# Kernel optimization log

Hardware: AMD Instinct MI355X
Metric: run time of the kernel (lower is better)

The kernel has to match this reference:

```python
import jax, jax.numpy as jnp
import numpy as np

B, N, C = 256, 256, 128   # batch (=N_res rows), seq len, pair channels
H, D = 4, 128             # heads, per-head dim (== output_dim per module code)
O = 128                   # output_dim


def _glorot(key, shape, fan_in, fan_out):
    limit = np.sqrt(6.0 / (fan_in + fan_out))
    return jax.random.uniform(key, shape, jnp.float32, -limit, limit)


def setup_inputs() -> dict:
    key = jax.random.key(0)
    ks = jax.random.split(key, 9)
    q_data = jax.random.normal(ks[0], (B, N, C), jnp.float32)
    m_data = jax.random.normal(ks[1], (B, N, C), jnp.float32)
    bias = jax.random.normal(ks[2], (B, 1, N, N), jnp.float32)
    nonbatched_bias = jax.random.normal(ks[3], (H, N, N), jnp.float32)
    query_w = _glorot(ks[4], (C, H, D), C, H * D)
    key_w = _glorot(ks[5], (C, H, D), C, H * D)
    value_w = _glorot(ks[6], (C, H, D), C, H * D)
    gating_w = jnp.zeros((C, H, D), jnp.float32)
    gating_b = jnp.ones((H, D), jnp.float32)
    output_w = _glorot(ks[7], (H, D, O), H * D, O)
    output_b = jnp.zeros((O,), jnp.float32)
    return {
        'q_data': q_data, 'm_data': m_data, 'bias': bias,
        'nonbatched_bias': nonbatched_bias,
        'query_w': query_w, 'key_w': key_w, 'value_w': value_w,
        'gating_w': gating_w, 'gating_b': gating_b,
        'output_w': output_w, 'output_b': output_b,
    }


def reference(q_data, m_data, bias, nonbatched_bias,
              query_w, key_w, value_w, gating_w, gating_b,
              output_w, output_b):
    key_dim = query_w.shape[-1]  # per-head dim (tied to output_dim in module)
    q = jnp.einsum('bqa,ahc->bqhc', q_data, query_w) * key_dim ** (-0.5)
    k = jnp.einsum('bka,ahc->bkhc', m_data, key_w)
    v = jnp.einsum('bka,ahc->bkhc', m_data, value_w)
    logits = jnp.einsum('bqhc,bkhc->bhqk', q, k) + bias
    logits = logits + nonbatched_bias[None]  # broadcast shared bias over batch
    weights = jax.nn.softmax(logits, axis=-1)
    weighted_avg = jnp.einsum('bhqk,bkhc->bqhc', weights, v)
    gate = jax.nn.sigmoid(jnp.einsum('bqc,chv->bqhv', q_data, gating_w) + gating_b)
    weighted_avg = weighted_avg * gate
    return jnp.einsum('bqhc,hco->bqo', weighted_avg, output_w) + output_b
```

## Files before the change

kernel.cpp:

```cpp
#include <hip/hip_runtime.h>
#include <stdint.h>


typedef unsigned short u16;
typedef u16 u16x8 __attribute__((ext_vector_type(8)));
typedef u16 u16x4 __attribute__((ext_vector_type(4)));
typedef __bf16 bf16x8 __attribute__((ext_vector_type(8)));
typedef float floatx4 __attribute__((ext_vector_type(4)));

union B8 { u16x8 u; bf16x8 b; };

__device__ __forceinline__ float bf2f(u16 u) {
  union { uint32_t i; float f; } v; v.i = ((uint32_t)u) << 16; return v.f;
}
__device__ __forceinline__ u16 f2bf(float f) {
  union { float f; uint32_t i; } v; v.f = f;
  return (u16)((v.i + 0x7fffu + ((v.i >> 16) & 1u)) >> 16);
}
__device__ __forceinline__ bf16x8 ld8(const u16* p) { return *(const bf16x8*)p; }
__device__ __forceinline__ floatx4 mfma16(bf16x8 a, bf16x8 b, floatx4 c) {
  return __builtin_amdgcn_mfma_f32_16x16x32_bf16(a, b, c, 0, 0, 0);
}
__device__ __forceinline__ void cfence() { asm volatile("" ::: "memory"); }

template<bool BF>
__device__ __forceinline__ bf16x8 ldin8(const void* p, long long idx) {
  if constexpr (BF) {
    return *(const bf16x8*)((const u16*)p + idx);
  } else {
    const float* f = (const float*)p + idx;
    floatx4 a = *(const floatx4*)f;
    floatx4 b = *(const floatx4*)(f + 4);
    B8 r;
    #pragma unroll
    for (int i = 0; i < 4; ++i) { r.u[i] = f2bf(a[i]); r.u[i + 4] = f2bf(b[i]); }
    return r.b;
  }
}
template<bool BF>
__device__ __forceinline__ float ldin1(const void* p, long long idx) {
  if constexpr (BF) return bf2f(((const u16*)p)[idx]);
  else              return ((const float*)p)[idx];
}

template<bool BF>
__device__ __forceinline__ void pre_body(
    const void* bias, const void* nbias,
    const void* qw, const void* kw, const void* vw, const void* gw,
    const void* ow, u16* wt, u16* b16, u16* nb16)
{
  const int blk = blockIdx.x, tid = threadIdx.x;
  if (blk < 4160) {
    const void* src = (blk < 4096) ? bias : nbias;
    u16* dst = (blk < 4096) ? b16 : nb16;
    long long base = (long long)((blk < 4096) ? blk : blk - 4096) * 4096;
    #pragma unroll
    for (int it = 0; it < 4; ++it) {
      long long idx = base + it * 1024 + tid * 4;
      if constexpr (BF) {
        *(u16x4*)(dst + idx) = *(const u16x4*)((const u16*)src + idx);
      } else {
        floatx4 v = *(const floatx4*)((const float*)src + idx);
        u16x4 o;
        #pragma unroll
        for (int i = 0; i < 4; ++i) o[i] = f2bf(v[i]);
        *(u16x4*)(dst + idx) = o;
      }
    }
  } else if (blk < 4176) {
    const int mh = blk - 4160, mat = mh >> 2, h = mh & 3;
    const void* W = (mat == 0) ? qw : (mat == 1) ? kw : (mat == 2) ? vw : gw;
    u16* dst = wt + mh * 16384;
    for (int idx = tid; idx < 16384; idx += 256) {
      int c = idx >> 7, d = idx & 127;
      dst[d * 128 + c] = f2bf(ldin1<BF>(W, (long long)c * 512 + h * 128 + d));
    }
  } else {
    const int part = blk - 4176;
    u16* dst = wt + 16 * 16384;
    for (int idx = tid; idx < 16384; idx += 256) {
      int k = idx >> 7, o = idx & 127;
      int kg = part * 128 + k;
      dst[o * 512 + kg] = f2bf(ldin1<BF>(ow, (long long)kg * 128 + o));
    }
  }
}

__global__ __launch_bounds__(256) void k_pre(
    const void* bias, const void* nbias,
    const void* qw, const void* kw, const void* vw, const void* gw,
    const void* ow, const void* gating_b, u16* wt, u16* b16, u16* nb16)
{
  const bool bf = (*(const uint32_t*)gating_b) == 0x3F803F80u;
  if (bf) pre_body<true >(bias, nbias, qw, kw, vw, gw, ow, wt, b16, nb16);
  else    pre_body<false>(bias, nbias, qw, kw, vw, gw, ow, wt, b16, nb16);
}

template<bool BF>
__device__ __forceinline__ void proj_body(
    const void* q_data, const void* m_data,
    const u16* wt, u16* reg, int b0, int Bc)
{
  const int tid  = threadIdx.x;
  const int lane = tid & 63, w = tid >> 6;
  const int quad = lane >> 4, l15 = lane & 15;
  const int mat  = blockIdx.y >> 2, h = blockIdx.y & 3;
  const int r0l  = blockIdx.x * 128;
  const int bl   = r0l >> 8, n0 = r0l & 255;
  const int bg   = b0 + bl;
  const long long regElems = (long long)Bc * 131072;

  const void* src = (mat == 0) ? q_data : m_data;
  const u16*  Wt  = wt + (mat * 4 + h) * 16384;

  const int wm = w >> 1, wn = w & 1;
  floatx4 acc[4][4];
  #pragma unroll
  for (int mi = 0; mi < 4; ++mi)
    #pragma unroll
    for (int ni = 0; ni < 4; ++ni)
      acc[mi][ni] = (floatx4){0.f, 0.f, 0.f, 0.f};

  #pragma unroll
  for (int ks = 0; ks < 4; ++ks) {
    bf16x8 af[4], bw[4];
    #pragma unroll
    for (int mi = 0; mi < 4; ++mi) {
      long long row = (long long)bg * 256 + n0 + wm * 64 + mi * 16 + l15;
      af[mi] = ldin8<BF>(src, row * 128 + ks * 32 + quad * 8);
    }
    #pragma unroll
    for (int ni = 0; ni < 4; ++ni) {
      int col = wn * 64 + ni * 16 + l15;
      bw[ni] = ld8(Wt + col * 128 + ks * 32 + quad * 8);
    }
    #pragma unroll
    for (int mi = 0; mi < 4; ++mi)
      #pragma unroll
      for (int ni = 0; ni < 4; ++ni)
        acc[mi][ni] = mfma16(af[mi], bw[ni], acc[mi][ni]);
  }

  const float scale = 0.088388347648318447f;
  const long long bh = (long long)(bl * 4 + h);
  #pragma unroll
  for (int mi = 0; mi < 4; ++mi) {
    #pragma unroll
    for (int ni = 0; ni < 4; ++ni) {
      if (mat == 2) {
        int j = wn * 64 + ni * 16 + l15;
        int i0 = wm * 64 + mi * 16 + quad * 4;
        u16x4 v4;
        #pragma unroll
        for (int r = 0; r < 4; ++r) v4[r] = f2bf(acc[mi][ni][r]);
        *(u16x4*)(reg + 2 * regElems + (bh * 128 + j) * 256 + (n0 + i0)) = v4;
      } else {
        #pragma unroll
        for (int r = 0; r < 4; ++r) {
          int i = wm * 64 + mi * 16 + quad * 4 + r;
          int j = wn * 64 + ni * 16 + l15;
          float v = acc[mi][ni][r];
          if (mat == 0) v *= scale;
          reg[(long long)mat * regElems + (bh * 256 + (n0 + i)) * 128 + j] = f2bf(v);
        }
      }
    }
  }
}

__global__ __launch_bounds__(256) void k_proj(
    const void* q_data, const void* m_data, const void* gating_b,
    const u16* wt, u16* reg, int b0, int Bc)
{
  const bool bf = (*(const uint32_t*)gating_b) == 0x3F803F80u;
  if (bf) proj_body<true >(q_data, m_data, wt, reg, b0, Bc);
  else    proj_body<false>(q_data, m_data, wt, reg, b0, Bc);
}

template<bool BF>
__device__ __forceinline__ void attn_body(
    const void* q_data, const u16* __restrict__ b16,
    const u16* __restrict__ nb16, const void* gating_b,
    const u16* __restrict__ wt, u16* reg, int b0, int Bc, char* smem)
{
  const int tid  = threadIdx.x;
  const int lane = tid & 63, w = tid >> 6;
  const int quad = lane >> 4, l15 = lane & 15;
  const int bl = blockIdx.x, h = blockIdx.y, qt = blockIdx.z;
  const int bg = b0 + bl;
  const int m0 = qt * 64 + w * 16;
  const long long regElems = (long long)Bc * 131072;
  const long long bh = (long long)(bl * 4 + h);

  const u16* Qb = reg;
  const u16* Kb = reg + regElems     + bh * 32768;
  const u16* Vt = reg + 2 * regElems + bh * 32768;
  u16*       Ob = reg + 3 * regElems;
  const u16* wtG = wt + (3 * 4 + h) * 16384;

  char* scr = smem + w * 4352;

  bf16x8 aq[4];
  #pragma unroll
  for (int ks = 0; ks < 4; ++ks)
    aq[ks] = ld8(Qb + (bh * 256 + m0 + l15) * 128 + ks * 32 + quad * 8);

  floatx4 s[16];
  #pragma unroll
  for (int nt = 0; nt < 16; ++nt) s[nt] = (floatx4){0.f, 0.f, 0.f, 0.f};

  #pragma unroll
  for (int kc = 0; kc < 4; ++kc) {
    float* sBf = (float*)scr;
    #pragma unroll
    for (int it = 0; it < 4; ++it) {
      int slot = it * 64 + lane;
      int row = slot >> 4, c4 = (slot & 15) << 2;
      long long gi = ((long long)bg * 256 + m0 + row) * 256 + kc * 64 + c4;
      long long ni = ((long long)h  * 256 + m0 + row) * 256 + kc * 64 + c4;
      u16x4 bu = *(const u16x4*)(b16 + gi);
      u16x4 nu = *(const u16x4*)(nb16 + ni);
      floatx4 v;
      #pragma unroll
      for (int i = 0; i < 4; ++i) v[i] = bf2f(bu[i]) + bf2f(nu[i]);
      *(floatx4*)(sBf + row * 68 + c4) = v;
    }
    #pragma unroll
    for (int ntl = 0; ntl < 4; ++ntl) {
      const int nt = kc * 4 + ntl;
      #pragma unroll
      for (int ks = 0; ks < 4; ++ks) {
        bf16x8 bk = ld8(Kb + (kc * 64 + ntl * 16 + l15) * 128 + ks * 32 + quad * 8);
        s[nt] = mfma16(aq[ks], bk, s[nt]);
      }
      #pragma unroll
      for (int r = 0; r < 4; ++r)
        s[nt][r] += sBf[(quad * 4 + r) * 68 + ntl * 16 + l15];
    }
    cfence();
  }

  float mx[4] = {-1e30f, -1e30f, -1e30f, -1e30f};
  #pragma unroll
  for (int nt = 0; nt < 16; ++nt)
    #pragma unroll
    for (int r = 0; r < 4; ++r) mx[r] = fmaxf(mx[r], s[nt][r]);
  #pragma unroll
  for (int r = 0; r < 4; ++r)
    #pragma unroll
    for (int off = 1; off < 16; off <<= 1)
      mx[r] = fmaxf(mx[r], __shfl_xor(mx[r], off));
  float sm[4] = {0.f, 0.f, 0.f, 0.f};
  #pragma unroll
  for (int nt = 0; nt < 16; ++nt)
    #pragma unroll
    for (int r = 0; r < 4; ++r) {
      float e = __expf(s[nt][r] - mx[r]);
      s[nt][r] = e; sm[r] += e;
    }
  #pragma unroll
  for (int r = 0; r < 4; ++r)
    #pragma unroll
    for (int off = 1; off < 16; off <<= 1)
      sm[r] += __shfl_xor(sm[r], off);
  float inv[4];
  #pragma unroll
  for (int r = 0; r < 4; ++r) inv[r] = 1.f / sm[r];

  u16* sPw = (u16*)scr;
  floatx4 o[8];
  #pragma unroll
  for (int dt = 0; dt < 8; ++dt) o[dt] = (floatx4){0.f, 0.f, 0.f, 0.f};
  #pragma unroll
  for (int half = 0; half < 2; ++half) {
    #pragma unroll
    for (int ntl = 0; ntl < 8; ++ntl)
      #pragma unroll
      for (int r = 0; r < 4; ++r)
        sPw[(quad * 4 + r) * 136 + ntl * 16 + l15] =
            f2bf(s[half * 8 + ntl][r] * inv[r]);
    bf16x8 ap[4];
    #pragma unroll
    for (int ks = 0; ks < 4; ++ks)
      ap[ks] = ld8(sPw + l15 * 136 + ks * 32 + quad * 8);
    #pragma unroll
    for (int dt = 0; dt < 8; ++dt)
      #pragma unroll
      for (int ks = 0; ks < 4; ++ks) {
        bf16x8 bv = ld8(Vt + (dt * 16 + l15) * 256 + half * 128 + ks * 32 + quad * 8);
        o[dt] = mfma16(ap[ks], bv, o[dt]);
      }
    cfence();
  }

  bf16x8 aqd[4];
  #pragma unroll
  for (int ks = 0; ks < 4; ++ks)
    aqd[ks] = ldin8<BF>(q_data, ((long long)bg * 256 + m0 + l15) * 128 + ks * 32 + quad * 8);
  #pragma unroll
  for (int nt = 0; nt < 8; ++nt) {
    floatx4 g = (floatx4){0.f, 0.f, 0.f, 0.f};
    #pragma unroll
    for (int ks = 0; ks < 4; ++ks) {
      bf16x8 bw = ld8(wtG + (nt * 16 + l15) * 128 + ks * 32 + quad * 8);
      g = mfma16(aqd[ks], bw, g);
    }
    #pragma unroll
    for (int r = 0; r < 4; ++r) {
      int row = m0 + quad * 4 + r, d = nt * 16 + l15;
      float gate = 1.f / (1.f + __expf(-(g[r] + ldin1<BF>(gating_b, h * 128 + d))));
      Ob[(bh * 256 + row) * 128 + d] = f2bf(o[nt][r] * gate);
    }
  }
}

__global__ __launch_bounds__(256, 4) void k_attn(
    const void* q_data, const u16* b16, const u16* nb16,
    const void* gating_b, const u16* wt, u16* reg, int b0, int Bc)
{
  __shared__ __align__(16) char smem[17408];
  const bool bf = (*(const uint32_t*)gating_b) == 0x3F803F80u;
  if (bf) attn_body<true >(q_data, b16, nb16, gating_b, wt, reg, b0, Bc, smem);
  else    attn_body<false>(q_data, b16, nb16, gating_b, wt, reg, b0, Bc, smem);
}

template<bool BF>
__device__ __forceinline__ void out_body(
    const u16* wsr, const u16* wtO, const void* output_b,
    void* out, int b0)
{
  const int tid  = threadIdx.x;
  const int lane = tid & 63, w = tid >> 6;
  const int quad = lane >> 4, l15 = lane & 15;
  const int wm = w >> 1, wn = w & 1;
  const int r0l = blockIdx.x * 32;
  const int bl  = r0l >> 8, n0 = r0l & 255;

  floatx4 acc[4];
  #pragma unroll
  for (int ni = 0; ni < 4; ++ni) acc[ni] = (floatx4){0.f, 0.f, 0.f, 0.f};

  #pragma unroll
  for (int kt = 0; kt < 4; ++kt) {
    #pragma unroll
    for (int ks = 0; ks < 4; ++ks) {
      bf16x8 af = ld8(wsr + ((long long)(bl * 4 + kt) * 256 + n0 + wm * 16 + l15) * 128
                          + ks * 32 + quad * 8);
      #pragma unroll
      for (int ni = 0; ni < 4; ++ni) {
        int col = wn * 64 + ni * 16 + l15;
        bf16x8 bw = ld8(wtO + (long long)col * 512 + kt * 128 + ks * 32 + quad * 8);
        acc[ni] = mfma16(af, bw, acc[ni]);
      }
    }
  }

  #pragma unroll
  for (int ni = 0; ni < 4; ++ni) {
    #pragma unroll
    for (int r = 0; r < 4; ++r) {
      int i = wm * 16 + quad * 4 + r;
      int j = wn * 64 + ni * 16 + l15;
      long long orow = (long long)b0 * 256 + r0l + i;
      float v = acc[ni][r] + ldin1<BF>(output_b, j);
      if constexpr (BF) ((u16*)out)[orow * 128 + j] = f2bf(v);
      else              ((float*)out)[orow * 128 + j] = v;
    }
  }
}

__global__ __launch_bounds__(256) void k_out(
    const u16* wsr, const u16* wtO, const void* output_b,
    const void* gating_b, void* out, int b0)
{
  const bool bf = (*(const uint32_t*)gating_b) == 0x3F803F80u;
  if (bf) out_body<true >(wsr, wtO, output_b, out, b0);
  else    out_body<false>(wsr, wtO, output_b, out, b0);
}

extern "C" void kernel_launch(void* const* d_in, const int* in_sizes, int n_in,
                              void* d_out, int out_size, void* d_ws, size_t ws_size,
                              hipStream_t stream)
{
  (void)in_sizes; (void)n_in; (void)out_size;
  const void* q_data   = d_in[0];
  const void* m_data   = d_in[1];
  const void* bias     = d_in[2];
  const void* nbias    = d_in[3];
  const void* query_w  = d_in[4];
  const void* key_w    = d_in[5];
  const void* value_w  = d_in[6];
  const void* gating_w = d_in[7];
  const void* gating_b = d_in[8];
  const void* output_w = d_in[9];
  const void* output_b = d_in[10];
  u16* ws = (u16*)d_ws;

  const long long wtElems  = 16 * 16384 + 128 * 512;
  const long long b16Elems = 256LL * 256 * 256;
  const long long nbElems  = 4LL * 256 * 256;
  const long long fixedElems = wtElems + b16Elems + nbElems;
  u16* wt   = ws;
  u16* wtO  = wt + 16 * 16384;
  u16* b16  = ws + wtElems;
  u16* nb16 = b16 + b16Elems;
  u16* reg  = ws + fixedElems;

  const size_t per_batch_bytes = 4ull * 131072 * 2;
  const size_t fixed_bytes = (size_t)fixedElems * 2;
  int Bc = 1;
  while (Bc * 2 <= 256 &&
         fixed_bytes + (size_t)(Bc * 2) * per_batch_bytes <= ws_size) Bc *= 2;

  k_pre<<<4180, 256, 0, stream>>>(bias, nbias, query_w, key_w, value_w,
                                  gating_w, output_w, gating_b, wt, b16, nb16);

  const long long regElems = (long long)Bc * 131072;
  for (int b0 = 0; b0 < 256; b0 += Bc) {
    dim3 g1(2 * Bc, 12);
    k_proj<<<g1, 256, 0, stream>>>(q_data, m_data, gating_b, wt, reg, b0, Bc);
    dim3 g2(Bc, 4, 4);
    k_attn<<<g2, 256, 0, stream>>>(q_data, b16, nb16, gating_b, wt, reg, b0, Bc);
    dim3 g3(8 * Bc);
    k_out<<<g3, 256, 0, stream>>>(reg + 3 * regElems, wtO, output_b,
                                  gating_b, d_out, b0);
  }
}
```

Measured before the change: 775.0 us.

## Read bias directly in attention instead of pre-converting to bf16 workspace

Removes the pre-pass that converted the full 64MB fp32 bias to a bf16 copy in workspace, and instead has the attention kernel load the bias in its native dtype directly. This eliminates a full read+write pass over the largest input, at the cost of the attention kernel reading fp32 (twice the bytes of the bf16 copy). It also flattens the attention grid to 1D with an XCD-style swizzle of block ids so that neighbouring work lands on the same chiplet, and frees workspace, which may allow a larger batch chunk.

```diff
diff --git a/kernel.cpp b/kernel.cpp
--- a/kernel.cpp
+++ b/kernel.cpp
@@ -45,30 +45,28 @@
 
 template<bool BF>
 __device__ __forceinline__ void pre_body(
-    const void* bias, const void* nbias,
+    const void* nbias,
     const void* qw, const void* kw, const void* vw, const void* gw,
-    const void* ow, u16* wt, u16* b16, u16* nb16)
+    const void* ow, u16* wt, u16* nb16)
 {
   const int blk = blockIdx.x, tid = threadIdx.x;
-  if (blk < 4160) {
-    const void* src = (blk < 4096) ? bias : nbias;
-    u16* dst = (blk < 4096) ? b16 : nb16;
-    long long base = (long long)((blk < 4096) ? blk : blk - 4096) * 4096;
+  if (blk < 64) {
+    long long base = (long long)blk * 4096;
     #pragma unroll
     for (int it = 0; it < 4; ++it) {
       long long idx = base + it * 1024 + tid * 4;
       if constexpr (BF) {
-        *(u16x4*)(dst + idx) = *(const u16x4*)((const u16*)src + idx);
+        *(u16x4*)(nb16 + idx) = *(const u16x4*)((const u16*)nbias + idx);
       } else {
-        floatx4 v = *(const floatx4*)((const float*)src + idx);
+        floatx4 v = *(const floatx4*)((const float*)nbias + idx);
         u16x4 o;
         #pragma unroll
         for (int i = 0; i < 4; ++i) o[i] = f2bf(v[i]);
-        *(u16x4*)(dst + idx) = o;
-      }
-    }
-  } else if (blk < 4176) {
-    const int mh = blk - 4160, mat = mh >> 2, h = mh & 3;
+        *(u16x4*)(nb16 + idx) = o;
+      }
+    }
+  } else if (blk < 80) {
+    const int mh = blk - 64, mat = mh >> 2, h = mh & 3;
     const void* W = (mat == 0) ? qw : (mat == 1) ? kw : (mat == 2) ? vw : gw;
     u16* dst = wt + mh * 16384;
     for (int idx = tid; idx < 16384; idx += 256) {
@@ -76,7 +74,7 @@
       dst[d * 128 + c] = f2bf(ldin1<BF>(W, (long long)c * 512 + h * 128 + d));
     }
   } else {
-    const int part = blk - 4176;
+    const int part = blk - 80;
     u16* dst = wt + 16 * 16384;
     for (int idx = tid; idx < 16384; idx += 256) {
       int k = idx >> 7, o = idx & 127;
@@ -87,13 +85,13 @@
 }
 
 __global__ __launch_bounds__(256) void k_pre(
-    const void* bias, const void* nbias,
+    const void* nbias,
     const void* qw, const void* kw, const void* vw, const void* gw,
-    const void* ow, const void* gating_b, u16* wt, u16* b16, u16* nb16)
+    const void* ow, const void* gating_b, u16* wt, u16* nb16)
 {
   const bool bf = (*(const uint32_t*)gating_b) == 0x3F803F80u;
-  if (bf) pre_body<true >(bias, nbias, qw, kw, vw, gw, ow, wt, b16, nb16);
-  else    pre_body<false>(bias, nbias, qw, kw, vw, gw, ow, wt, b16, nb16);
+  if (bf) pre_body<true >(nbias, qw, kw, vw, gw, ow, wt, nb16);
+  else    pre_body<false>(nbias, qw, kw, vw, gw, ow, wt, nb16);
 }
 
 template<bool BF>
@@ -179,14 +177,20 @@
 
 template<bool BF>
 __device__ __forceinline__ void attn_body(
-    const void* q_data, const u16* __restrict__ b16,
+    const void* q_data, const void* __restrict__ bias,
     const u16* __restrict__ nb16, const void* gating_b,
     const u16* __restrict__ wt, u16* reg, int b0, int Bc, char* smem)
 {
   const int tid  = threadIdx.x;
   const int lane = tid & 63, w = tid >> 6;
   const int quad = lane >> 4, l15 = lane & 15;
-  const int bl = blockIdx.x, h = blockIdx.y, qt = blockIdx.z;
+
+  const int nwg = Bc * 16;
+  const int id  = blockIdx.x;
+  const int per = nwg >> 3;
+  const int swz = (id & 7) * per + (id >> 3);
+  const int bl = swz >> 4, h = (swz >> 2) & 3, qt = swz & 3;
+
   const int bg = b0 + bl;
   const int m0 = qt * 64 + w * 16;
   const long long regElems = (long long)Bc * 131072;
@@ -218,11 +222,17 @@
       int row = slot >> 4, c4 = (slot & 15) << 2;
       long long gi = ((long long)bg * 256 + m0 + row) * 256 + kc * 64 + c4;
       long long ni = ((long long)h  * 256 + m0 + row) * 256 + kc * 64 + c4;
-      u16x4 bu = *(const u16x4*)(b16 + gi);
       u16x4 nu = *(const u16x4*)(nb16 + ni);
       floatx4 v;
-      #pragma unroll
-      for (int i = 0; i < 4; ++i) v[i] = bf2f(bu[i]) + bf2f(nu[i]);
+      if constexpr (BF) {
+        u16x4 bu = *(const u16x4*)((const u16*)bias + gi);
+        #pragma unroll
+        for (int i = 0; i < 4; ++i) v[i] = bf2f(bu[i]) + bf2f(nu[i]);
+      } else {
+        floatx4 bv = *(const floatx4*)((const float*)bias + gi);
+        #pragma unroll
+        for (int i = 0; i < 4; ++i) v[i] = bv[i] + bf2f(nu[i]);
+      }
       *(floatx4*)(sBf + row * 68 + c4) = v;
     }
     #pragma unroll
@@ -315,13 +325,13 @@
 }
 
 __global__ __launch_bounds__(256, 4) void k_attn(
-    const void* q_data, const u16* b16, const u16* nb16,
+    const void* q_data, const void* bias, const u16* nb16,
     const void* gating_b, const u16* wt, u16* reg, int b0, int Bc)
 {
   __shared__ __align__(16) char smem[17408];
   const bool bf = (*(const uint32_t*)gating_b) == 0x3F803F80u;
-  if (bf) attn_body<true >(q_data, b16, nb16, gating_b, wt, reg, b0, Bc, smem);
-  else    attn_body<false>(q_data, b16, nb16, gating_b, wt, reg, b0, Bc, smem);
+  if (bf) attn_body<true >(q_data, bias, nb16, gating_b, wt, reg, b0, Bc, smem);
+  else    attn_body<false>(q_data, bias, nb16, gating_b, wt, reg, b0, Bc, smem);
 }
 
 template<bool BF>
@@ -397,13 +407,11 @@
   u16* ws = (u16*)d_ws;
 
   const long long wtElems  = 16 * 16384 + 128 * 512;
-  const long long b16Elems = 256LL * 256 * 256;
   const long long nbElems  = 4LL * 256 * 256;
-  const long long fixedElems = wtElems + b16Elems + nbElems;
+  const long long fixedElems = wtElems + nbElems;
   u16* wt   = ws;
   u16* wtO  = wt + 16 * 16384;
-  u16* b16  = ws + wtElems;
-  u16* nb16 = b16 + b16Elems;
+  u16* nb16 = ws + wtElems;
   u16* reg  = ws + fixedElems;
 
   const size_t per_batch_bytes = 4ull * 131072 * 2;
@@ -412,15 +420,15 @@
   while (Bc * 2 <= 256 &&
          fixed_bytes + (size_t)(Bc * 2) * per_batch_bytes <= ws_size) Bc *= 2;
 
-  k_pre<<<4180, 256, 0, stream>>>(bias, nbias, query_w, key_w, value_w,
-                                  gating_w, output_w, gating_b, wt, b16, nb16);
+  k_pre<<<84, 256, 0, stream>>>(nbias, query_w, key_w, value_w,
+                                gating_w, output_w, gating_b, wt, nb16);
 
   const long long regElems = (long long)Bc * 131072;
   for (int b0 = 0; b0 < 256; b0 += Bc) {
     dim3 g1(2 * Bc, 12);
     k_proj<<<g1, 256, 0, stream>>>(q_data, m_data, gating_b, wt, reg, b0, Bc);
-    dim3 g2(Bc, 4, 4);
-    k_attn<<<g2, 256, 0, stream>>>(q_data, b16, nb16, gating_b, wt, reg, b0, Bc);
+    k_attn<<<Bc * 16, 256, 0, stream>>>(q_data, bias, nb16, gating_b, wt,
+                                        reg, b0, Bc);
     dim3 g3(8 * Bc);
     k_out<<<g3, 256, 0, stream>>>(reg + 3 * regElems, wtO, output_b,
                                   gating_b, d_out, b0);
```

After: 769.3 us. About the same (-0.7%).

## Fuse QKV projection, attention and gating into one kernel with LDS-resident K/V

Applied to the files above, without the earlier changes.

Merges the projection and attention kernels into a single 512-thread workgroup per (batch, head). It computes Q, K and V on chip, keeps K and transposed V in swizzled LDS, and reads the fp32 bias and nonbatched bias directly instead of pre-converting them to bf16 in a separate pass. This removes the global round trip of Q/K/V, the big bias conversion kernel, and one launch per chunk. It also adds an XCD-aware block swizzle and defers the softmax normalisation to the output. In exchange it uses about 146KB of LDS per block, which limits occupancy, and it issues scalar fp32 bias loads.

```diff
diff --git a/kernel.cpp b/kernel.cpp
--- a/kernel.cpp
+++ b/kernel.cpp
@@ -45,38 +45,20 @@
 
 template<bool BF>
 __device__ __forceinline__ void pre_body(
-    const void* bias, const void* nbias,
     const void* qw, const void* kw, const void* vw, const void* gw,
-    const void* ow, u16* wt, u16* b16, u16* nb16)
+    const void* ow, u16* wt)
 {
   const int blk = blockIdx.x, tid = threadIdx.x;
-  if (blk < 4160) {
-    const void* src = (blk < 4096) ? bias : nbias;
-    u16* dst = (blk < 4096) ? b16 : nb16;
-    long long base = (long long)((blk < 4096) ? blk : blk - 4096) * 4096;
-    #pragma unroll
-    for (int it = 0; it < 4; ++it) {
-      long long idx = base + it * 1024 + tid * 4;
-      if constexpr (BF) {
-        *(u16x4*)(dst + idx) = *(const u16x4*)((const u16*)src + idx);
-      } else {
-        floatx4 v = *(const floatx4*)((const float*)src + idx);
-        u16x4 o;
-        #pragma unroll
-        for (int i = 0; i < 4; ++i) o[i] = f2bf(v[i]);
-        *(u16x4*)(dst + idx) = o;
-      }
-    }
-  } else if (blk < 4176) {
-    const int mh = blk - 4160, mat = mh >> 2, h = mh & 3;
+  if (blk < 16) {
+    const int mat = blk >> 2, h = blk & 3;
     const void* W = (mat == 0) ? qw : (mat == 1) ? kw : (mat == 2) ? vw : gw;
-    u16* dst = wt + mh * 16384;
+    u16* dst = wt + blk * 16384;
     for (int idx = tid; idx < 16384; idx += 256) {
       int c = idx >> 7, d = idx & 127;
       dst[d * 128 + c] = f2bf(ldin1<BF>(W, (long long)c * 512 + h * 128 + d));
     }
   } else {
-    const int part = blk - 4176;
+    const int part = blk - 16;
     u16* dst = wt + 16 * 16384;
     for (int idx = tid; idx < 16384; idx += 256) {
       int k = idx >> 7, o = idx & 127;
@@ -87,241 +69,256 @@
 }
 
 __global__ __launch_bounds__(256) void k_pre(
-    const void* bias, const void* nbias,
     const void* qw, const void* kw, const void* vw, const void* gw,
-    const void* ow, const void* gating_b, u16* wt, u16* b16, u16* nb16)
+    const void* ow, const void* gating_b, u16* wt)
 {
   const bool bf = (*(const uint32_t*)gating_b) == 0x3F803F80u;
-  if (bf) pre_body<true >(bias, nbias, qw, kw, vw, gw, ow, wt, b16, nb16);
-  else    pre_body<false>(bias, nbias, qw, kw, vw, gw, ow, wt, b16, nb16);
+  if (bf) pre_body<true >(qw, kw, vw, gw, ow, wt);
+  else    pre_body<false>(qw, kw, vw, gw, ow, wt);
 }
 
 template<bool BF>
-__device__ __forceinline__ void proj_body(
+__device__ __forceinline__ void fused_body(
     const void* q_data, const void* m_data,
-    const u16* wt, u16* reg, int b0, int Bc)
+    const void* __restrict__ bias, const void* __restrict__ nbias,
+    const void* gating_b, const u16* __restrict__ wt,
+    u16* Ob, int b0, int Bc, u16* smem)
 {
   const int tid  = threadIdx.x;
   const int lane = tid & 63, w = tid >> 6;
   const int quad = lane >> 4, l15 = lane & 15;
-  const int mat  = blockIdx.y >> 2, h = blockIdx.y & 3;
-  const int r0l  = blockIdx.x * 128;
-  const int bl   = r0l >> 8, n0 = r0l & 255;
-  const int bg   = b0 + bl;
-  const long long regElems = (long long)Bc * 131072;
-
-  const void* src = (mat == 0) ? q_data : m_data;
-  const u16*  Wt  = wt + (mat * 4 + h) * 16384;
-
-  const int wm = w >> 1, wn = w & 1;
-  floatx4 acc[4][4];
+  const int l7   = l15 & 7;
+
+  const int nwg = Bc * 4, id = blockIdx.x;
+  const int xcd = id & 7, rest = id >> 3;
+  const int qq = nwg >> 3, rm = nwg & 7;
+  const int swz = (xcd < rm ? xcd * (qq + 1) : rm * (qq + 1) + (xcd - rm) * qq) + rest;
+  const int bl = swz >> 2, h = swz & 3;
+  const int bg = b0 + bl;
+  const long long bh = (long long)(bl * 4 + h);
+
+  u16* Kl  = smem;
+  u16* Vtl = Kl + 32768;
+  u16* sPw = Vtl + 32768 + w * 1152;
+
+  const u16* wtQ = wt + (0 * 4 + h) * 16384;
+  const u16* wtK = wt + (1 * 4 + h) * 16384;
+  const u16* wtV = wt + (2 * 4 + h) * 16384;
+  const u16* wtG = wt + (3 * 4 + h) * 16384;
+  const float scale = 0.088388347648318447f;
+
+  bf16x8 aq[2][4];
+  u16* Qs = Kl + w * 4096;
   #pragma unroll
-  for (int mi = 0; mi < 4; ++mi)
-    #pragma unroll
-    for (int ni = 0; ni < 4; ++ni)
-      acc[mi][ni] = (floatx4){0.f, 0.f, 0.f, 0.f};
+  for (int p = 0; p < 2; ++p) {
+    const int m0 = p * 128 + w * 16;
+    floatx4 qa[8];
+    #pragma unroll
+    for (int ni = 0; ni < 8; ++ni) qa[ni] = (floatx4){0.f, 0.f, 0.f, 0.f};
+    #pragma unroll
+    for (int ks = 0; ks < 4; ++ks) {
+      bf16x8 aA = ldin8<BF>(q_data, ((long long)bg * 256 + m0 + l15) * 128 + ks * 32 + quad * 8);
+      #pragma unroll
+      for (int ni = 0; ni < 8; ++ni) {
+        bf16x8 bw = ld8(wtQ + (ni * 16 + l15) * 128 + ks * 32 + quad * 8);
+        qa[ni] = mfma16(aA, bw, qa[ni]);
+      }
+    }
+    #pragma unroll
+    for (int ni = 0; ni < 8; ++ni)
+      #pragma unroll
+      for (int r = 0; r < 4; ++r)
+        Qs[(quad * 4 + r) * 136 + ni * 16 + l15] = f2bf(qa[ni][r] * scale);
+    cfence();
+    #pragma unroll
+    for (int ks = 0; ks < 4; ++ks)
+      aq[p][ks] = ld8(Qs + l15 * 136 + ks * 32 + quad * 8);
+    cfence();
+  }
+  __syncthreads();
+
+  const int nb = w * 32;
+  {
+    floatx4 ka[2][8];
+    #pragma unroll
+    for (int mi = 0; mi < 2; ++mi)
+      #pragma unroll
+      for (int ni = 0; ni < 8; ++ni) ka[mi][ni] = (floatx4){0.f, 0.f, 0.f, 0.f};
+    #pragma unroll
+    for (int ks = 0; ks < 4; ++ks) {
+      bf16x8 bw[8];
+      #pragma unroll
+      for (int ni = 0; ni < 8; ++ni)
+        bw[ni] = ld8(wtK + (ni * 16 + l15) * 128 + ks * 32 + quad * 8);
+      #pragma unroll
+      for (int mi = 0; mi < 2; ++mi) {
+        bf16x8 aA = ldin8<BF>(m_data, ((long long)bg * 256 + nb + mi * 16 + l15) * 128 + ks * 32 + quad * 8);
+        #pragma unroll
+        for (int ni = 0; ni < 8; ++ni)
+          ka[mi][ni] = mfma16(aA, bw[ni], ka[mi][ni]);
+      }
+    }
+    #pragma unroll
+    for (int mi = 0; mi < 2; ++mi)
+      #pragma unroll
+      for (int ni = 0; ni < 8; ++ni)
+        #pragma unroll
+        for (int r = 0; r < 4; ++r) {
+          int n = nb + mi * 16 + quad * 4 + r;
+          int d = ni * 16 + l15;
+          Kl[n * 128 + (d ^ ((n & 7) << 3))] = f2bf(ka[mi][ni][r]);
+        }
+  }
+  {
+    floatx4 va[2][8];
+    #pragma unroll
+    for (int mi = 0; mi < 2; ++mi)
+      #pragma unroll
+      for (int ni = 0; ni < 8; ++ni) va[mi][ni] = (floatx4){0.f, 0.f, 0.f, 0.f};
+    #pragma unroll
+    for (int ks = 0; ks < 4; ++ks) {
+      bf16x8 bw[8];
+      #pragma unroll
+      for (int ni = 0; ni < 8; ++ni)
+        bw[ni] = ld8(wtV + (ni * 16 + l15) * 128 + ks * 32 + quad * 8);
+      #pragma unroll
+      for (int mi = 0; mi < 2; ++mi) {
+        bf16x8 aA = ldin8<BF>(m_data, ((long long)bg * 256 + nb + mi * 16 + l15) * 128 + ks * 32 + quad * 8);
+        #pragma unroll
+        for (int ni = 0; ni < 8; ++ni)
+          va[mi][ni] = mfma16(aA, bw[ni], va[mi][ni]);
+      }
+    }
+    #pragma unroll
+    for (int mi = 0; mi < 2; ++mi)
+      #pragma unroll
+      for (int ni = 0; ni < 8; ++ni) {
+        int d = ni * 16 + l15;
+        int n4 = nb + mi * 16 + quad * 4;
+        u16x4 v4;
+        #pragma unroll
+        for (int r = 0; r < 4; ++r) v4[r] = f2bf(va[mi][ni][r]);
+        *(u16x4*)(Vtl + d * 256 + (n4 ^ ((d & 7) << 3))) = v4;
+      }
+  }
+  __syncthreads();
 
   #pragma unroll
-  for (int ks = 0; ks < 4; ++ks) {
-    bf16x8 af[4], bw[4];
-    #pragma unroll
-    for (int mi = 0; mi < 4; ++mi) {
-      long long row = (long long)bg * 256 + n0 + wm * 64 + mi * 16 + l15;
-      af[mi] = ldin8<BF>(src, row * 128 + ks * 32 + quad * 8);
-    }
-    #pragma unroll
-    for (int ni = 0; ni < 4; ++ni) {
-      int col = wn * 64 + ni * 16 + l15;
-      bw[ni] = ld8(Wt + col * 128 + ks * 32 + quad * 8);
-    }
-    #pragma unroll
-    for (int mi = 0; mi < 4; ++mi)
-      #pragma unroll
-      for (int ni = 0; ni < 4; ++ni)
-        acc[mi][ni] = mfma16(af[mi], bw[ni], acc[mi][ni]);
-  }
-
-  const float scale = 0.088388347648318447f;
-  const long long bh = (long long)(bl * 4 + h);
-  #pragma unroll
-  for (int mi = 0; mi < 4; ++mi) {
-    #pragma unroll
-    for (int ni = 0; ni < 4; ++ni) {
-      if (mat == 2) {
-        int j = wn * 64 + ni * 16 + l15;
-        int i0 = wm * 64 + mi * 16 + quad * 4;
-        u16x4 v4;
-        #pragma unroll
-        for (int r = 0; r < 4; ++r) v4[r] = f2bf(acc[mi][ni][r]);
-        *(u16x4*)(reg + 2 * regElems + (bh * 128 + j) * 256 + (n0 + i0)) = v4;
-      } else {
+  for (int p = 0; p < 2; ++p) {
+    const int m0 = p * 128 + w * 16;
+
+    floatx4 s[16];
+    #pragma unroll
+    for (int nt = 0; nt < 16; ++nt) s[nt] = (floatx4){0.f, 0.f, 0.f, 0.f};
+    #pragma unroll
+    for (int kc = 0; kc < 4; ++kc) {
+      float bz[4][4];
+      #pragma unroll
+      for (int ntl = 0; ntl < 4; ++ntl)
         #pragma unroll
         for (int r = 0; r < 4; ++r) {
-          int i = wm * 64 + mi * 16 + quad * 4 + r;
-          int j = wn * 64 + ni * 16 + l15;
-          float v = acc[mi][ni][r];
-          if (mat == 0) v *= scale;
-          reg[(long long)mat * regElems + (bh * 256 + (n0 + i)) * 128 + j] = f2bf(v);
+          long long gi = ((long long)bg * 256 + m0 + quad * 4 + r) * 256 + kc * 64 + ntl * 16 + l15;
+          long long gn = ((long long)h * 256 + m0 + quad * 4 + r) * 256 + kc * 64 + ntl * 16 + l15;
+          bz[ntl][r] = ldin1<BF>(bias, gi) + ldin1<BF>(nbias, gn);
         }
-      }
-    }
-  }
-}
-
-__global__ __launch_bounds__(256) void k_proj(
-    const void* q_data, const void* m_data, const void* gating_b,
-    const u16* wt, u16* reg, int b0, int Bc)
-{
+      #pragma unroll
+      for (int ntl = 0; ntl < 4; ++ntl) {
+        const int nt = kc * 4 + ntl;
+        #pragma unroll
+        for (int ks = 0; ks < 4; ++ks) {
+          bf16x8 bk = ld8(Kl + (kc * 64 + ntl * 16 + l15) * 128 +
+                          ((ks * 32 + quad * 8) ^ (l7 << 3)));
+          s[nt] = mfma16(aq[p][ks], bk, s[nt]);
+        }
+        #pragma unroll
+        for (int r = 0; r < 4; ++r) s[nt][r] += bz[ntl][r];
+      }
+    }
+
+    float mx[4] = {-1e30f, -1e30f, -1e30f, -1e30f};
+    #pragma unroll
+    for (int nt = 0; nt < 16; ++nt)
+      #pragma unroll
+      for (int r = 0; r < 4; ++r) mx[r] = fmaxf(mx[r], s[nt][r]);
+    #pragma unroll
+    for (int r = 0; r < 4; ++r)
+      #pragma unroll
+      for (int off = 1; off < 16; off <<= 1)
+        mx[r] = fmaxf(mx[r], __shfl_xor(mx[r], off));
+    float sm[4] = {0.f, 0.f, 0.f, 0.f};
+    #pragma unroll
+    for (int nt = 0; nt < 16; ++nt)
+      #pragma unroll
+      for (int r = 0; r < 4; ++r) {
+        float e = __expf(s[nt][r] - mx[r]);
+        s[nt][r] = e; sm[r] += e;
+      }
+    #pragma unroll
+    for (int r = 0; r < 4; ++r)
+      #pragma unroll
+      for (int off = 1; off < 16; off <<= 1)
+        sm[r] += __shfl_xor(sm[r], off);
+    float inv[4];
+    #pragma unroll
+    for (int r = 0; r < 4; ++r) inv[r] = 1.f / sm[r];
+
+    floatx4 o[8];
+    #pragma unroll
+    for (int dt = 0; dt < 8; ++dt) o[dt] = (floatx4){0.f, 0.f, 0.f, 0.f};
+    #pragma unroll
+    for (int c = 0; c < 4; ++c) {
+      #pragma unroll
+      for (int ntl = 0; ntl < 4; ++ntl)
+        #pragma unroll
+        for (int r = 0; r < 4; ++r)
+          sPw[(quad * 4 + r) * 72 + ntl * 16 + l15] = f2bf(s[c * 4 + ntl][r]);
+      cfence();
+      bf16x8 ap[2];
+      #pragma unroll
+      for (int k2 = 0; k2 < 2; ++k2)
+        ap[k2] = ld8(sPw + l15 * 72 + k2 * 32 + quad * 8);
+      #pragma unroll
+      for (int dt = 0; dt < 8; ++dt)
+        #pragma unroll
+        for (int k2 = 0; k2 < 2; ++k2) {
+          bf16x8 bv = ld8(Vtl + (dt * 16 + l15) * 256 +
+                          ((c * 64 + k2 * 32 + quad * 8) ^ (l7 << 3)));
+          o[dt] = mfma16(ap[k2], bv, o[dt]);
+        }
+      cfence();
+    }
+
+    bf16x8 aqd[4];
+    #pragma unroll
+    for (int ks = 0; ks < 4; ++ks)
+      aqd[ks] = ldin8<BF>(q_data, ((long long)bg * 256 + m0 + l15) * 128 + ks * 32 + quad * 8);
+    #pragma unroll
+    for (int nt = 0; nt < 8; ++nt) {
+      floatx4 g = (floatx4){0.f, 0.f, 0.f, 0.f};
+      #pragma unroll
+      for (int ks = 0; ks < 4; ++ks) {
+        bf16x8 bw = ld8(wtG + (nt * 16 + l15) * 128 + ks * 32 + quad * 8);
+        g = mfma16(aqd[ks], bw, g);
+      }
+      #pragma unroll
+      for (int r = 0; r < 4; ++r) {
+        int row = m0 + quad * 4 + r, d = nt * 16 + l15;
+        float gate = 1.f / (1.f + __expf(-(g[r] + ldin1<BF>(gating_b, h * 128 + d))));
+        Ob[(bh * 256 + row) * 128 + d] = f2bf(o[nt][r] * inv[r] * gate);
+      }
+    }
+  }
+}
+
+__global__ __launch_bounds__(512, 2) void k_fused(
+    const void* q_data, const void* m_data, const void* bias,
+    const void* nbias, const void* gating_b, const u16* wt,
+    u16* Ob, int b0, int Bc)
+{
+  __shared__ __align__(16) u16 smem[74752];
   const bool bf = (*(const uint32_t*)gating_b) == 0x3F803F80u;
-  if (bf) proj_body<true >(q_data, m_data, wt, reg, b0, Bc);
-  else    proj_body<false>(q_data, m_data, wt, reg, b0, Bc);
-}
-
-template<bool BF>
-__device__ __forceinline__ void attn_body(
-    const void* q_data, const u16* __restrict__ b16,
-    const u16* __restrict__ nb16, const void* gating_b,
-    const u16* __restrict__ wt, u16* reg, int b0, int Bc, char* smem)
-{
-  const int tid  = threadIdx.x;
-  const int lane = tid & 63, w = tid >> 6;
-  const int quad = lane >> 4, l15 = lane & 15;
-  const int bl = blockIdx.x, h = blockIdx.y, qt = blockIdx.z;
-  const int bg = b0 + bl;
-  const int m0 = qt * 64 + w * 16;
-  const long long regElems = (long long)Bc * 131072;
-  const long long bh = (long long)(bl * 4 + h);
-
-  const u16* Qb = reg;
-  const u16* Kb = reg + regElems     + bh * 32768;
-  const u16* Vt = reg + 2 * regElems + bh * 32768;
-  u16*       Ob = reg + 3 * regElems;
-  const u16* wtG = wt + (3 * 4 + h) * 16384;
-
-  char* scr = smem + w * 4352;
-
-  bf16x8 aq[4];
-  #pragma unroll
-  for (int ks = 0; ks < 4; ++ks)
-    aq[ks] = ld8(Qb + (bh * 256 + m0 + l15) * 128 + ks * 32 + quad * 8);
-
-  floatx4 s[16];
-  #pragma unroll
-  for (int nt = 0; nt < 16; ++nt) s[nt] = (floatx4){0.f, 0.f, 0.f, 0.f};
-
-  #pragma unroll
-  for (int kc = 0; kc < 4; ++kc) {
-    float* sBf = (float*)scr;
-    #pragma unroll
-    for (int it = 0; it < 4; ++it) {
-      int slot = it * 64 + lane;
-      int row = slot >> 4, c4 = (slot & 15) << 2;
-      long long gi = ((long long)bg * 256 + m0 + row) * 256 + kc * 64 + c4;
-      long long ni = ((long long)h  * 256 + m0 + row) * 256 + kc * 64 + c4;
-      u16x4 bu = *(const u16x4*)(b16 + gi);
-      u16x4 nu = *(const u16x4*)(nb16 + ni);
-      floatx4 v;
-      #pragma unroll
-      for (int i = 0; i < 4; ++i) v[i] = bf2f(bu[i]) + bf2f(nu[i]);
-      *(floatx4*)(sBf + row * 68 + c4) = v;
-    }
-    #pragma unroll
-    for (int ntl = 0; ntl < 4; ++ntl) {
-      const int nt = kc * 4 + ntl;
-      #pragma unroll
-      for (int ks = 0; ks < 4; ++ks) {
-        bf16x8 bk = ld8(Kb + (kc * 64 + ntl * 16 + l15) * 128 + ks * 32 + quad * 8);
-        s[nt] = mfma16(aq[ks], bk, s[nt]);
-      }
-      #pragma unroll
-      for (int r = 0; r < 4; ++r)
-        s[nt][r] += sBf[(quad * 4 + r) * 68 + ntl * 16 + l15];
-    }
-    cfence();
-  }
-
-  float mx[4] = {-1e30f, -1e30f, -1e30f, -1e30f};
-  #pragma unroll
-  for (int nt = 0; nt < 16; ++nt)
-    #pragma unroll
-    for (int r = 0; r < 4; ++r) mx[r] = fmaxf(mx[r], s[nt][r]);
-  #pragma unroll
-  for (int r = 0; r < 4; ++r)
-    #pragma unroll
-    for (int off = 1; off < 16; off <<= 1)
-      mx[r] = fmaxf(mx[r], __shfl_xor(mx[r], off));
-  float sm[4] = {0.f, 0.f, 0.f, 0.f};
-  #pragma unroll
-  for (int nt = 0; nt < 16; ++nt)
-    #pragma unroll
-    for (int r = 0; r < 4; ++r) {
-      float e = __expf(s[nt][r] - mx[r]);
-      s[nt][r] = e; sm[r] += e;
-    }
-  #pragma unroll
-  for (int r = 0; r < 4; ++r)
-    #pragma unroll
-    for (int off = 1; off < 16; off <<= 1)
-      sm[r] += __shfl_xor(sm[r], off);
-  float inv[4];
-  #pragma unroll
-  for (int r = 0; r < 4; ++r) inv[r] = 1.f / sm[r];
-
-  u16* sPw = (u16*)scr;
-  floatx4 o[8];
-  #pragma unroll
-  for (int dt = 0; dt < 8; ++dt) o[dt] = (floatx4){0.f, 0.f, 0.f, 0.f};
-  #pragma unroll
-  for (int half = 0; half < 2; ++half) {
-    #pragma unroll
-    for (int ntl = 0; ntl < 8; ++ntl)
-      #pragma unroll
-      for (int r = 0; r < 4; ++r)
-        sPw[(quad * 4 + r) * 136 + ntl * 16 + l15] =
-            f2bf(s[half * 8 + ntl][r] * inv[r]);
-    bf16x8 ap[4];
-    #pragma unroll
-    for (int ks = 0; ks < 4; ++ks)
-      ap[ks] = ld8(sPw + l15 * 136 + ks * 32 + quad * 8);
-    #pragma unroll
-    for (int dt = 0; dt < 8; ++dt)
-      #pragma unroll
-      for (int ks = 0; ks < 4; ++ks) {
-        bf16x8 bv = ld8(Vt + (dt * 16 + l15) * 256 + half * 128 + ks * 32 + quad * 8);
-        o[dt] = mfma16(ap[ks], bv, o[dt]);
-      }
-    cfence();
-  }
-
-  bf16x8 aqd[4];
-  #pragma unroll
-  for (int ks = 0; ks < 4; ++ks)
-    aqd[ks] = ldin8<BF>(q_data, ((long long)bg * 256 + m0 + l15) * 128 + ks * 32 + quad * 8);
-  #pragma unroll
-  for (int nt = 0; nt < 8; ++nt) {
-    floatx4 g = (floatx4){0.f, 0.f, 0.f, 0.f};
-    #pragma unroll
-    for (int ks = 0; ks < 4; ++ks) {
-      bf16x8 bw = ld8(wtG + (nt * 16 + l15) * 128 + ks * 32 + quad * 8);
-      g = mfma16(aqd[ks], bw, g);
-    }
-    #pragma unroll
-    for (int r = 0; r < 4; ++r) {
-      int row = m0 + quad * 4 + r, d = nt * 16 + l15;
-      float gate = 1.f / (1.f + __expf(-(g[r] + ldin1<BF>(gating_b, h * 128 + d))));
-      Ob[(bh * 256 + row) * 128 + d] = f2bf(o[nt][r] * gate);
-    }
-  }
-}
-
-__global__ __launch_bounds__(256, 4) void k_attn(
-    const void* q_data, const u16* b16, const u16* nb16,
-    const void* gating_b, const u16* wt, u16* reg, int b0, int Bc)
-{
-  __shared__ __align__(16) char smem[17408];
-  const bool bf = (*(const uint32_t*)gating_b) == 0x3F803F80u;
-  if (bf) attn_body<true >(q_data, b16, nb16, gating_b, wt, reg, b0, Bc, smem);
-  else    attn_body<false>(q_data, b16, nb16, gating_b, wt, reg, b0, Bc, smem);
+  if (bf) fused_body<true >(q_data, m_data, bias, nbias, gating_b, wt, Ob, b0, Bc, smem);
+  else    fused_body<false>(q_data, m_data, bias, nbias, gating_b, wt, Ob, b0, Bc, smem);
 }
 
 template<bool BF>
@@ -396,33 +393,24 @@
   const void* output_b = d_in[10];
   u16* ws = (u16*)d_ws;
 
-  const long long wtElems  = 16 * 16384 + 128 * 512;
-  const long long b16Elems = 256LL * 256 * 256;
-  const long long nbElems  = 4LL * 256 * 256;
-  const long long fixedElems = wtElems + b16Elems + nbElems;
-  u16* wt   = ws;
-  u16* wtO  = wt + 16 * 16384;
-  u16* b16  = ws + wtElems;
-  u16* nb16 = b16 + b16Elems;
-  u16* reg  = ws + fixedElems;
-
-  const size_t per_batch_bytes = 4ull * 131072 * 2;
-  const size_t fixed_bytes = (size_t)fixedElems * 2;
+  const long long wtElems = 16 * 16384 + 128 * 512;
+  u16* wt  = ws;
+  u16* wtO = wt + 16 * 16384;
+  u16* reg = ws + wtElems;
+
+  const size_t per_batch_bytes = 131072ull * 2;
+  const size_t fixed_bytes = (size_t)wtElems * 2;
   int Bc = 1;
   while (Bc * 2 <= 256 &&
          fixed_bytes + (size_t)(Bc * 2) * per_batch_bytes <= ws_size) Bc *= 2;
 
-  k_pre<<<4180, 256, 0, stream>>>(bias, nbias, query_w, key_w, value_w,
-                                  gating_w, output_w, gating_b, wt, b16, nb16);
-
-  const long long regElems = (long long)Bc * 131072;
+  k_pre<<<20, 256, 0, stream>>>(query_w, key_w, value_w, gating_w,
+                                output_w, gating_b, wt);
+
   for (int b0 = 0; b0 < 256; b0 += Bc) {
-    dim3 g1(2 * Bc, 12);
-    k_proj<<<g1, 256, 0, stream>>>(q_data, m_data, gating_b, wt, reg, b0, Bc);
-    dim3 g2(Bc, 4, 4);
-    k_attn<<<g2, 256, 0, stream>>>(q_data, b16, nb16, gating_b, wt, reg, b0, Bc);
-    dim3 g3(8 * Bc);
-    k_out<<<g3, 256, 0, stream>>>(reg + 3 * regElems, wtO, output_b,
-                                  gating_b, d_out, b0);
-  }
-}
+    k_fused<<<Bc * 4, 512, 0, stream>>>(q_data, m_data, bias, nbias,
+                                        gating_b, wt, reg, b0, Bc);
+    k_out<<<8 * Bc, 256, 0, stream>>>(reg, wtO, output_b,
+                                      gating_b, d_out, b0);
+  }
+}
```

Result: faster. 673.4 us (-13.1%).
